# Performance work log

Measured on AMD Instinct MI355X. Metric: run time of the kernel, lower is better.

The kernel has to match this reference:

```python
import jax, jax.numpy as jnp
import numpy as np

# Module hyper-parameters (eval mode: remove_rand_on_eval=True => no random additional points)
B, H, C, E = 2, 8, 2048, 1024
D = 64          # head_size
KP = 8          # k (points per query per head)
P = 2 * KP      # num_points = k * 2**rank, rank = 1


def setup_inputs() -> dict:
    key = jax.random.key(0)
    ks = jax.random.split(key, 10)
    x = jax.random.normal(ks[0], (B, C, E), jnp.float32)
    attention_mask = jnp.ones((B, C), jnp.int32)  # accepted but unused, as in the torch forward
    # hyper() outputs (abstract in the class): continuous means in [0, C-1), positive sigmas, values
    means = jax.random.uniform(ks[1], (B, H, C, KP, 1), jnp.float32) * (C - 1)
    sigmas = jax.random.uniform(ks[2], (B, H, C, KP), jnp.float32) * 2.0 + 0.5
    values = jax.random.normal(ks[3], (B, H, C, KP), jnp.float32)
    s_in = 1.0 / np.sqrt(E).astype(np.float32)
    s_u = 1.0 / np.sqrt(H * D).astype(np.float32)
    Wk = jax.random.normal(ks[4], (E, H * D), jnp.float32) * s_in
    Wq = jax.random.normal(ks[5], (E, H * D), jnp.float32) * s_in
    Wv = jax.random.normal(ks[6], (E, H * D), jnp.float32) * s_in
    Wu = jax.random.normal(ks[7], (H * D, E), jnp.float32) * s_u
    bu = jnp.zeros((E,), jnp.float32)
    return dict(x=x, attention_mask=attention_mask, means=means, sigmas=sigmas,
                values=values, Wk=Wk, Wq=Wq, Wv=Wv, Wu=Wu, bu=bu)


def reference(x, attention_mask, means, sigmas, values, Wk, Wq, Wv, Wu, bu):
    b, c, e = x.shape
    h, d, kp, p = H, D, KP, P

    # ---- ngenerate (eval: only the 2**rank = 2 integer corners per mean, clamped in-range) ----
    m = means[..., 0]                                  # (b,h,c,k)
    i0 = jnp.clip(jnp.floor(m).astype(jnp.int32), 0, c - 1)
    i1 = jnp.clip(i0 + 1, 0, c - 1)
    idx = jnp.stack([i0, i1], axis=-1).reshape(b, h, c, p)   # (b,h,c,P)
    idx_fl = idx.astype(jnp.float32)

    # ---- densities: unnormalized Gaussian of each integer point under each of the k means ----
    diff = idx_fl[..., :, None] - m[..., None, :]            # (b,h,c,P,k)
    dens = jnp.exp(-0.5 * (diff / sigmas[..., None, :]) ** 2)

    # ---- nduplicates: zero densities of repeated index tuples (keep first occurrence) ----
    eq = idx[..., :, None] == idx[..., None, :]              # (b,h,c,P,P)
    earlier = jnp.tril(jnp.ones((p, p), bool), k=-1)         # q < p
    dup = jnp.any(eq & earlier, axis=-1)                     # (b,h,c,P)
    dens = jnp.where(dup[..., None], 0.0, dens)

    # normalize over dim=2 (context), exactly as the torch code does
    dens = dens / (dens.sum(axis=2, keepdims=True) + 1e-8)

    # density-weighted continuous values -> per-point weights
    weights = (values[..., None, :] * dens).sum(axis=-1)     # (b,h,c,P)

    # ---- projections ----
    inv_sqrt_d = 1.0 / np.sqrt(d).astype(np.float32)
    Kt = (x @ Wk).reshape(b, c, h, d).transpose(0, 2, 1, 3) * inv_sqrt_d  # (b,h,c,d)
    Qt = (x @ Wq).reshape(b, c, h, d).transpose(0, 2, 1, 3) * inv_sqrt_d
    Vt = (x @ Wv).reshape(b, c, h, d).transpose(0, 2, 1, 3)

    # ---- gather K/V at the sparse indices ----
    flat = idx.reshape(b, h, c * p, 1)
    Kg = jnp.take_along_axis(Kt, flat, axis=2).reshape(b, h, c, p, d)
    Vg = jnp.take_along_axis(Vt, flat, axis=2).reshape(b, h, c, p, d)

    dots = jnp.einsum('bhcd,bhcpd->bhcp', Qt, Kg)
    new_weights = jax.nn.softmax(weights * dots, axis=-1)    # (b,h,c,P)

    head_reps = jnp.einsum('bhcpd,bhcp->bhcd', Vg, new_weights)
    united = head_reps.transpose(0, 2, 1, 3).reshape(b, c, h * d)
    new_out = united @ Wu + bu

    # ---- scatter-add sparse weights into dense attention matrix ----
    bi = jnp.arange(b)[:, None, None, None]
    hi = jnp.arange(h)[None, :, None, None]
    ci = jnp.arange(c)[None, None, :, None]
    attentions = jnp.zeros((b, h, c, c), jnp.float32).at[bi, hi, ci, idx].add(new_weights)

    return new_out, attentions
```

## Files before the change

kernel.cpp:

```cpp
#include <hip/hip_runtime.h>
#include <math.h>
#include <stdint.h>

#define B_ 2
#define H_ 8
#define C_ 2048
#define E_ 1024
#define D_ 64
#define KP_ 8
#define P_ 16
#define HD_ 512
#define ROWS_ 32768
#define M_ 4096

typedef __bf16 bf16x8 __attribute__((ext_vector_type(8)));
typedef float f32x4 __attribute__((ext_vector_type(4)));
typedef uint16_t u16x8 __attribute__((ext_vector_type(8)));

__device__ inline uint16_t f2bf(float f) {
    union { float f; uint32_t u; } v; v.f = f;
    uint32_t u = v.u + 0x7FFF + ((v.u >> 16) & 1);
    return (uint16_t)(u >> 16);
}
__device__ inline float bf2f(uint16_t h) {
    union { uint32_t u; float f; } v; v.u = ((uint32_t)h) << 16;
    return v.f;
}

__device__ inline void gload16(const uint16_t* g, uint16_t* l) {
    __builtin_amdgcn_global_load_lds(
        (const __attribute__((address_space(1))) void*)g,
        (__attribute__((address_space(3))) void*)l, 16, 0, 0);
}

__global__ __launch_bounds__(256) void convert_x_kernel(
    const float* __restrict__ in, uint16_t* __restrict__ out)
{
    const int i = (blockIdx.x * 256 + threadIdx.x) * 8;
    const float4 a = *(const float4*)(in + i);
    const float4 b = *(const float4*)(in + i + 4);
    u16x8 o;
    o[0] = f2bf(a.x); o[1] = f2bf(a.y); o[2] = f2bf(a.z); o[3] = f2bf(a.w);
    o[4] = f2bf(b.x); o[5] = f2bf(b.y); o[6] = f2bf(b.z); o[7] = f2bf(b.w);
    *(u16x8*)(out + i) = o;
}

__global__ __launch_bounds__(256) void convert_wt_kernel(
    const float* __restrict__ Wq, const float* __restrict__ Wk,
    const float* __restrict__ Wv, const float* __restrict__ Wu,
    uint16_t* __restrict__ Wqt, uint16_t* __restrict__ Wkt,
    uint16_t* __restrict__ Wvt, uint16_t* __restrict__ Wut)
{
    const int z = blockIdx.z;
    const float* in; uint16_t* out; int R, Cc;
    if (z == 0)      { in = Wq; out = Wqt; R = E_;  Cc = HD_; }
    else if (z == 1) { in = Wk; out = Wkt; R = E_;  Cc = HD_; }
    else if (z == 2) { in = Wv; out = Wvt; R = E_;  Cc = HD_; }
    else             { in = Wu; out = Wut; R = HD_; Cc = E_; }
    const int tiles_x = Cc >> 5;
    const int tx = blockIdx.x % tiles_x;
    const int ty = blockIdx.x / tiles_x;
    const int r0 = ty * 32, c0 = tx * 32;
    __shared__ float t[32][33];
    const int lx = threadIdx.x & 31, ly = threadIdx.x >> 5;
#pragma unroll
    for (int i = 0; i < 4; ++i)
        t[ly * 4 + i][lx] = in[(size_t)(r0 + ly * 4 + i) * Cc + c0 + lx];
    __syncthreads();
#pragma unroll
    for (int i = 0; i < 4; ++i)
        out[(size_t)(c0 + ly * 4 + i) * R + r0 + lx] = f2bf(t[lx][ly * 4 + i]);
}

__global__ __launch_bounds__(256) void gemm_qkv_kernel(
    const uint16_t* __restrict__ xb,
    const uint16_t* __restrict__ Wqt, const uint16_t* __restrict__ Wkt,
    const uint16_t* __restrict__ Wvt,
    uint16_t* __restrict__ Qt, uint16_t* __restrict__ Kt,
    uint16_t* __restrict__ Vt)
{
    const int z = blockIdx.z;
    const uint16_t* __restrict__ Wt = (z == 0) ? Wqt : (z == 1) ? Wkt : Wvt;
    uint16_t* __restrict__ Out = (z == 0) ? Qt : (z == 1) ? Kt : Vt;
    const float scale = (z == 2) ? 1.0f : 0.125f;
    const int K = E_;
    const int m0 = blockIdx.y * 128;
    const int n0 = blockIdx.x * 128;

    __shared__ __align__(16) uint16_t As[128 * 32];
    __shared__ __align__(16) uint16_t Bs[128 * 32];

    const int tid = threadIdx.x;
    const int w = tid >> 6, lane = tid & 63;
    const int wm = w & 1, wn = w >> 1;

    f32x4 acc[4][4] = {};

    const int r0s = (w * 2 + 0) * 16 + (lane >> 2);
    const int r1s = (w * 2 + 1) * 16 + (lane >> 2);
    const int ko  = (lane & 3) * 8;
    const uint16_t* gA0 = xb + (size_t)(m0 + r0s) * K + ko;
    const uint16_t* gA1 = xb + (size_t)(m0 + r1s) * K + ko;
    const uint16_t* gB0 = Wt + (size_t)(n0 + r0s) * K + ko;
    const uint16_t* gB1 = Wt + (size_t)(n0 + r1s) * K + ko;
    uint16_t* lA0 = &As[(w * 2 + 0) * 512];
    uint16_t* lA1 = &As[(w * 2 + 1) * 512];
    uint16_t* lB0 = &Bs[(w * 2 + 0) * 512];
    uint16_t* lB1 = &Bs[(w * 2 + 1) * 512];

    const int fr = lane & 15;
    const int fk = (lane >> 4) * 8;

    for (int k0 = 0; k0 < K; k0 += 32) {
        __syncthreads();
        gload16(gA0 + k0, lA0);
        gload16(gA1 + k0, lA1);
        gload16(gB0 + k0, lB0);
        gload16(gB1 + k0, lB1);
        __syncthreads();
        bf16x8 af[4], bf[4];
#pragma unroll
        for (int t = 0; t < 4; ++t) {
            af[t] = *(const bf16x8*)&As[(wm * 64 + t * 16 + fr) * 32 + fk];
            bf[t] = *(const bf16x8*)&Bs[(wn * 64 + t * 16 + fr) * 32 + fk];
        }
#pragma unroll
        for (int mt = 0; mt < 4; ++mt)
#pragma unroll
            for (int nt = 0; nt < 4; ++nt)
                acc[mt][nt] = __builtin_amdgcn_mfma_f32_16x16x32_bf16(
                    af[mt], bf[nt], acc[mt][nt], 0, 0, 0);
    }

#pragma unroll
    for (int mt = 0; mt < 4; ++mt) {
#pragma unroll
        for (int nt = 0; nt < 4; ++nt) {
            const int n = n0 + wn * 64 + nt * 16 + fr;
            const int h = n >> 6, d = n & 63;
#pragma unroll
            for (int r = 0; r < 4; ++r) {
                const int m = m0 + wm * 64 + mt * 16 + (lane >> 4) * 4 + r;
                const int b = m >> 11, c = m & (C_ - 1);
                Out[(((size_t)(b * H_ + h) * C_ + c) << 6) + d] =
                    f2bf(acc[mt][nt][r] * scale);
            }
        }
    }
}

__global__ __launch_bounds__(256) void gemm_out_kernel(
    const uint16_t* __restrict__ U, const uint16_t* __restrict__ Wut,
    const float* __restrict__ bu, float* __restrict__ out)
{
    const int K = HD_;
    const int m0 = blockIdx.y * 128;
    const int n0 = blockIdx.x * 128;

    __shared__ __align__(16) uint16_t As[128 * 32];
    __shared__ __align__(16) uint16_t Bs[128 * 32];

    const int tid = threadIdx.x;
    const int w = tid >> 6, lane = tid & 63;
    const int wm = w & 1, wn = w >> 1;

    f32x4 acc[4][4] = {};

    const int r0s = (w * 2 + 0) * 16 + (lane >> 2);
    const int r1s = (w * 2 + 1) * 16 + (lane >> 2);
    const int ko  = (lane & 3) * 8;
    const uint16_t* gA0 = U + (size_t)(m0 + r0s) * K + ko;
    const uint16_t* gA1 = U + (size_t)(m0 + r1s) * K + ko;
    const uint16_t* gB0 = Wut + (size_t)(n0 + r0s) * K + ko;
    const uint16_t* gB1 = Wut + (size_t)(n0 + r1s) * K + ko;
    uint16_t* lA0 = &As[(w * 2 + 0) * 512];
    uint16_t* lA1 = &As[(w * 2 + 1) * 512];
    uint16_t* lB0 = &Bs[(w * 2 + 0) * 512];
    uint16_t* lB1 = &Bs[(w * 2 + 1) * 512];

    const int fr = lane & 15;
    const int fk = (lane >> 4) * 8;

    for (int k0 = 0; k0 < K; k0 += 32) {
        __syncthreads();
        gload16(gA0 + k0, lA0);
        gload16(gA1 + k0, lA1);
        gload16(gB0 + k0, lB0);
        gload16(gB1 + k0, lB1);
        __syncthreads();
        bf16x8 af[4], bf[4];
#pragma unroll
        for (int t = 0; t < 4; ++t) {
            af[t] = *(const bf16x8*)&As[(wm * 64 + t * 16 + fr) * 32 + fk];
            bf[t] = *(const bf16x8*)&Bs[(wn * 64 + t * 16 + fr) * 32 + fk];
        }
#pragma unroll
        for (int mt = 0; mt < 4; ++mt)
#pragma unroll
            for (int nt = 0; nt < 4; ++nt)
                acc[mt][nt] = __builtin_amdgcn_mfma_f32_16x16x32_bf16(
                    af[mt], bf[nt], acc[mt][nt], 0, 0, 0);
    }

#pragma unroll
    for (int mt = 0; mt < 4; ++mt) {
#pragma unroll
        for (int nt = 0; nt < 4; ++nt) {
            const int n = n0 + wn * 64 + nt * 16 + fr;
            const float bias = bu[n];
#pragma unroll
            for (int r = 0; r < 4; ++r) {
                const int m = m0 + wm * 64 + mt * 16 + (lane >> 4) * 4 + r;
                out[(size_t)m * E_ + n] = acc[mt][nt][r] + bias;
            }
        }
    }
}

__global__ __launch_bounds__(256) void dens_sum_kernel(
    const float* __restrict__ means, const float* __restrict__ sigmas,
    float* __restrict__ S)
{
    const int row = blockIdx.x * 256 + threadIdx.x;
    const int lane = threadIdx.x & 63;
    const int bh = row >> 11;

    const float* mrow = means + (size_t)row * 8;
    const float* srow = sigmas + (size_t)row * 8;
    const float4 ma = *(const float4*)(mrow);
    const float4 mb = *(const float4*)(mrow + 4);
    const float4 sa = *(const float4*)(srow);
    const float4 sb = *(const float4*)(srow + 4);
    const float mm[8] = {ma.x, ma.y, ma.z, ma.w, mb.x, mb.y, mb.z, mb.w};
    const float sg[8] = {sa.x, sa.y, sa.z, sa.w, sb.x, sb.y, sb.z, sb.w};

    int idx[16];
#pragma unroll
    for (int j = 0; j < 8; ++j) {
        int i0 = (int)floorf(mm[j]);
        i0 = min(max(i0, 0), C_ - 1);
        idx[2 * j] = i0;
        idx[2 * j + 1] = min(i0 + 1, C_ - 1);
    }
    unsigned dupm = 0;
#pragma unroll
    for (int p = 1; p < 16; ++p) {
        bool d = false;
#pragma unroll
        for (int q = 0; q < 15; ++q)
            if (q < p) d = d || (idx[q] == idx[p]);
        if (d) dupm |= (1u << p);
    }

#pragma unroll
    for (int p = 0; p < 16; ++p) {
        const float fi = (float)idx[p];
        const bool dup = (dupm >> p) & 1u;
#pragma unroll
        for (int kk = 0; kk < 8; ++kk) {
            const float t = (fi - mm[kk]) / sg[kk];
            float val = dup ? 0.0f : expf(-0.5f * t * t);
#pragma unroll
            for (int off = 1; off < 64; off <<= 1)
                val += __shfl_xor(val, off);
            if (lane == 0)
                atomicAdd(&S[bh * 128 + p * 8 + kk], val);
        }
    }
}

__global__ __launch_bounds__(256) void attn_kernel(
    const float* __restrict__ means, const float* __restrict__ sigmas,
    const float* __restrict__ values, const float* __restrict__ S,
    const uint16_t* __restrict__ Qt, const uint16_t* __restrict__ Kt,
    const uint16_t* __restrict__ Vt, uint16_t* __restrict__ united,
    float* __restrict__ attn)
{
    __shared__ float rowbuf[4][2048];
    const int w = threadIdx.x >> 6;
    const int lane = threadIdx.x & 63;
    const int row = blockIdx.x * 4 + w;
    const int bh = row >> 11;
    const int c = row & (C_ - 1);
    const int b = bh >> 3;
    const int h = bh & 7;

    const float* mrow = means + (size_t)row * 8;
    const float4 ma = *(const float4*)(mrow);
    const float4 mb = *(const float4*)(mrow + 4);
    const float mm[8] = {ma.x, ma.y, ma.z, ma.w, mb.x, mb.y, mb.z, mb.w};

    int idx[16];
#pragma unroll
    for (int j = 0; j < 8; ++j) {
        int i0 = (int)floorf(mm[j]);
        i0 = min(max(i0, 0), C_ - 1);
        idx[2 * j] = i0;
        idx[2 * j + 1] = min(i0 + 1, C_ - 1);
    }

    const int lp = lane & 15;
    int myidx = 0;
#pragma unroll
    for (int q = 0; q < 16; ++q)
        if (q == lp) myidx = idx[q];
    float wp = 0.0f;
    if (lane < 16) {
        bool dup = false;
#pragma unroll
        for (int q = 0; q < 15; ++q)
            dup = dup || ((q < lane) && (idx[q] == myidx));
        if (!dup) {
            const float* srow = sigmas + (size_t)row * 8;
            const float* vrow = values + (size_t)row * 8;
            const float4 sa = *(const float4*)(srow);
            const float4 sb = *(const float4*)(srow + 4);
            const float4 va = *(const float4*)(vrow);
            const float4 vb = *(const float4*)(vrow + 4);
            const float sg[8] = {sa.x, sa.y, sa.z, sa.w, sb.x, sb.y, sb.z, sb.w};
            const float vl[8] = {va.x, va.y, va.z, va.w, vb.x, vb.y, vb.z, vb.w};
            const float* Sp = S + bh * 128 + lane * 8;
            const float4 Sa = *(const float4*)(Sp);
            const float4 Sb = *(const float4*)(Sp + 4);
            const float Sv[8] = {Sa.x, Sa.y, Sa.z, Sa.w, Sb.x, Sb.y, Sb.z, Sb.w};
            const float fi = (float)myidx;
#pragma unroll
            for (int kk = 0; kk < 8; ++kk) {
                const float t = (fi - mm[kk]) / sg[kk];
                const float e = expf(-0.5f * t * t);
                wp = fmaf(vl[kk], e / (Sv[kk] + 1e-8f), wp);
            }
        }
    }

    const int p = lane >> 2, g = lane & 3;
    int kidx = 0;
#pragma unroll
    for (int q = 0; q < 16; ++q)
        if (q == p) kidx = idx[q];

    const uint16_t* Qrow = Qt + ((size_t)row << 6);
    const uint16_t* Krow = Kt + ((((size_t)bh << 11) + kidx) << 6);
    const u16x8 qa = *(const u16x8*)(Qrow + g * 16);
    const u16x8 qb = *(const u16x8*)(Qrow + g * 16 + 8);
    const u16x8 ka = *(const u16x8*)(Krow + g * 16);
    const u16x8 kb = *(const u16x8*)(Krow + g * 16 + 8);
    float dot = 0.0f;
#pragma unroll
    for (int j = 0; j < 8; ++j) {
        dot = fmaf(bf2f(qa[j]), bf2f(ka[j]), dot);
        dot = fmaf(bf2f(qb[j]), bf2f(kb[j]), dot);
    }
    dot += __shfl_xor(dot, 1);
    dot += __shfl_xor(dot, 2);

    const float wvp = __shfl(wp, p);
    const float logit = wvp * dot;

    float mx = logit;
#pragma unroll
    for (int off = 4; off < 64; off <<= 1)
        mx = fmaxf(mx, __shfl_xor(mx, off));
    const float e = expf(logit - mx);
    float se = e;
#pragma unroll
    for (int off = 4; off < 64; off <<= 1)
        se += __shfl_xor(se, off);
    const float sm = e / se;

    float smv[16];
#pragma unroll
    for (int q = 0; q < 16; ++q)
        smv[q] = __shfl(sm, q * 4);

    const uint16_t* Vbh = Vt + ((size_t)bh << 17);
    float acc = 0.0f;
#pragma unroll
    for (int q = 0; q < 16; ++q)
        acc = fmaf(bf2f(Vbh[((size_t)idx[q] << 6) + lane]), smv[q], acc);
    united[((size_t)(b * C_ + c)) * HD_ + h * 64 + lane] = f2bf(acc);

    const float4 z4 = make_float4(0.f, 0.f, 0.f, 0.f);
#pragma unroll
    for (int j = 0; j < 8; ++j)
        *(float4*)&rowbuf[w][(j * 64 + lane) * 4] = z4;
    __syncthreads();
    if (lane < 16) atomicAdd(&rowbuf[w][myidx], smv[lane]);
    __syncthreads();
    float* arow = attn + ((size_t)row << 11);
#pragma unroll
    for (int j = 0; j < 8; ++j) {
        const int o = (j * 64 + lane) * 4;
        *(float4*)&arow[o] = *(const float4*)&rowbuf[w][o];
    }
}

extern "C" void kernel_launch(void* const* d_in, const int* in_sizes, int n_in,
                              void* d_out, int out_size, void* d_ws,
                              size_t ws_size, hipStream_t stream) {
    const float* x      = (const float*)d_in[0];
    const float* means  = (const float*)d_in[2];
    const float* sigmas = (const float*)d_in[3];
    const float* values = (const float*)d_in[4];
    const float* Wk     = (const float*)d_in[5];
    const float* Wq     = (const float*)d_in[6];
    const float* Wv     = (const float*)d_in[7];
    const float* Wu     = (const float*)d_in[8];
    const float* bu     = (const float*)d_in[9];

    float* out  = (float*)d_out;
    float* attn = out + (size_t)M_ * E_;

    uint16_t* wsp = (uint16_t*)d_ws;
    uint16_t* xb     = wsp;
    uint16_t* Wqt    = xb + 4194304;
    uint16_t* Wkt    = Wqt + 524288;
    uint16_t* Wvt    = Wkt + 524288;
    uint16_t* Wut    = Wvt + 524288;
    uint16_t* Qt     = Wut + 524288;
    uint16_t* Kt     = Qt + 2097152;
    uint16_t* Vt     = Kt + 2097152;
    uint16_t* united = Vt + 2097152;
    float*    S      = (float*)(united + 2097152);

    hipMemsetAsync(S, 0, 2048 * sizeof(float), stream);

    convert_x_kernel<<<2048, 256, 0, stream>>>(x, xb);
    convert_wt_kernel<<<dim3(512, 1, 4), 256, 0, stream>>>(
        Wq, Wk, Wv, Wu, Wqt, Wkt, Wvt, Wut);
    dens_sum_kernel<<<128, 256, 0, stream>>>(means, sigmas, S);
    gemm_qkv_kernel<<<dim3(4, 32, 3), 256, 0, stream>>>(
        xb, Wqt, Wkt, Wvt, Qt, Kt, Vt);
    attn_kernel<<<ROWS_ / 4, 256, 0, stream>>>(
        means, sigmas, values, S, Qt, Kt, Vt, united, attn);
    gemm_out_kernel<<<dim3(8, 32), 256, 0, stream>>>(united, Wut, bu, out);
}
```

Before: 423.9 us.

## Fuse QKV weights into one matrix, fold scale, write attention rows directly

The Q/K/V weight transposes are packed into one contiguous matrix, and the 1/sqrt(d) scale is folded into the weight conversion. The QKV GEMM becomes a single 12x32 grid that picks its output buffer from the column tile. The attention kernel drops its 32KB shared-memory row buffer and the two block barriers. It now zeroes each attention row with nontemporal global stores, issues a threadfence, then atomically adds the 16 softmax weights into global memory. This should raise occupancy and remove the LDS staging, but it depends on the zero stores being ordered before the global atomics, and it adds global atomic traffic.

```diff
diff --git a/kernel.cpp b/kernel.cpp
--- a/kernel.cpp
+++ b/kernel.cpp
@@ -48,15 +48,14 @@
 __global__ __launch_bounds__(256) void convert_wt_kernel(
     const float* __restrict__ Wq, const float* __restrict__ Wk,
     const float* __restrict__ Wv, const float* __restrict__ Wu,
-    uint16_t* __restrict__ Wqt, uint16_t* __restrict__ Wkt,
-    uint16_t* __restrict__ Wvt, uint16_t* __restrict__ Wut)
+    uint16_t* __restrict__ Wall, uint16_t* __restrict__ Wut)
 {
     const int z = blockIdx.z;
-    const float* in; uint16_t* out; int R, Cc;
-    if (z == 0)      { in = Wq; out = Wqt; R = E_;  Cc = HD_; }
-    else if (z == 1) { in = Wk; out = Wkt; R = E_;  Cc = HD_; }
-    else if (z == 2) { in = Wv; out = Wvt; R = E_;  Cc = HD_; }
-    else             { in = Wu; out = Wut; R = HD_; Cc = E_; }
+    const float* in; uint16_t* out; int R, Cc; float scale;
+    if (z == 0)      { in = Wq; out = Wall;                 R = E_;  Cc = HD_; scale = 0.125f; }
+    else if (z == 1) { in = Wk; out = Wall + 512 * 1024;    R = E_;  Cc = HD_; scale = 0.125f; }
+    else if (z == 2) { in = Wv; out = Wall + 1024 * 1024;   R = E_;  Cc = HD_; scale = 1.0f; }
+    else             { in = Wu; out = Wut;                  R = HD_; Cc = E_;  scale = 1.0f; }
     const int tiles_x = Cc >> 5;
     const int tx = blockIdx.x % tiles_x;
     const int ty = blockIdx.x / tiles_x;
@@ -69,23 +68,19 @@
     __syncthreads();
 #pragma unroll
     for (int i = 0; i < 4; ++i)
-        out[(size_t)(c0 + ly * 4 + i) * R + r0 + lx] = f2bf(t[lx][ly * 4 + i]);
+        out[(size_t)(c0 + ly * 4 + i) * R + r0 + lx] = f2bf(t[lx][ly * 4 + i] * scale);
 }
 
 __global__ __launch_bounds__(256) void gemm_qkv_kernel(
-    const uint16_t* __restrict__ xb,
-    const uint16_t* __restrict__ Wqt, const uint16_t* __restrict__ Wkt,
-    const uint16_t* __restrict__ Wvt,
+    const uint16_t* __restrict__ xb, const uint16_t* __restrict__ Wall,
     uint16_t* __restrict__ Qt, uint16_t* __restrict__ Kt,
     uint16_t* __restrict__ Vt)
 {
-    const int z = blockIdx.z;
-    const uint16_t* __restrict__ Wt = (z == 0) ? Wqt : (z == 1) ? Wkt : Wvt;
-    uint16_t* __restrict__ Out = (z == 0) ? Qt : (z == 1) ? Kt : Vt;
-    const float scale = (z == 2) ? 1.0f : 0.125f;
     const int K = E_;
     const int m0 = blockIdx.y * 128;
     const int n0 = blockIdx.x * 128;
+    const int z = n0 >> 9;
+    uint16_t* __restrict__ Out = (z == 0) ? Qt : (z == 1) ? Kt : Vt;
 
     __shared__ __align__(16) uint16_t As[128 * 32];
     __shared__ __align__(16) uint16_t Bs[128 * 32];
@@ -101,8 +96,8 @@
     const int ko  = (lane & 3) * 8;
     const uint16_t* gA0 = xb + (size_t)(m0 + r0s) * K + ko;
     const uint16_t* gA1 = xb + (size_t)(m0 + r1s) * K + ko;
-    const uint16_t* gB0 = Wt + (size_t)(n0 + r0s) * K + ko;
-    const uint16_t* gB1 = Wt + (size_t)(n0 + r1s) * K + ko;
+    const uint16_t* gB0 = Wall + (size_t)(n0 + r0s) * K + ko;
+    const uint16_t* gB1 = Wall + (size_t)(n0 + r1s) * K + ko;
     uint16_t* lA0 = &As[(w * 2 + 0) * 512];
     uint16_t* lA1 = &As[(w * 2 + 1) * 512];
     uint16_t* lB0 = &Bs[(w * 2 + 0) * 512];
@@ -136,14 +131,14 @@
     for (int mt = 0; mt < 4; ++mt) {
 #pragma unroll
         for (int nt = 0; nt < 4; ++nt) {
-            const int n = n0 + wn * 64 + nt * 16 + fr;
-            const int h = n >> 6, d = n & 63;
+            const int nl = (n0 & 511) + wn * 64 + nt * 16 + fr;
+            const int h = nl >> 6, d = nl & 63;
 #pragma unroll
             for (int r = 0; r < 4; ++r) {
                 const int m = m0 + wm * 64 + mt * 16 + (lane >> 4) * 4 + r;
                 const int b = m >> 11, c = m & (C_ - 1);
                 Out[(((size_t)(b * H_ + h) * C_ + c) << 6) + d] =
-                    f2bf(acc[mt][nt][r] * scale);
+                    f2bf(acc[mt][nt][r]);
             }
         }
     }
@@ -276,7 +271,6 @@
     const uint16_t* __restrict__ Vt, uint16_t* __restrict__ united,
     float* __restrict__ attn)
 {
-    __shared__ float rowbuf[4][2048];
     const int w = threadIdx.x >> 6;
     const int lane = threadIdx.x & 63;
     const int row = blockIdx.x * 4 + w;
@@ -372,6 +366,7 @@
 #pragma unroll
     for (int q = 0; q < 16; ++q)
         smv[q] = __shfl(sm, q * 4);
+    const float myw = __shfl(sm, lp * 4);
 
     const uint16_t* Vbh = Vt + ((size_t)bh << 17);
     float acc = 0.0f;
@@ -380,19 +375,13 @@
         acc = fmaf(bf2f(Vbh[((size_t)idx[q] << 6) + lane]), smv[q], acc);
     united[((size_t)(b * C_ + c)) * HD_ + h * 64 + lane] = f2bf(acc);
 
-    const float4 z4 = make_float4(0.f, 0.f, 0.f, 0.f);
+    float* arow = attn + ((size_t)row << 11);
+    const f32x4 z4 = {0.f, 0.f, 0.f, 0.f};
 #pragma unroll
     for (int j = 0; j < 8; ++j)
-        *(float4*)&rowbuf[w][(j * 64 + lane) * 4] = z4;
-    __syncthreads();
-    if (lane < 16) atomicAdd(&rowbuf[w][myidx], smv[lane]);
-    __syncthreads();
-    float* arow = attn + ((size_t)row << 11);
-#pragma unroll
-    for (int j = 0; j < 8; ++j) {
-        const int o = (j * 64 + lane) * 4;
-        *(float4*)&arow[o] = *(const float4*)&rowbuf[w][o];
-    }
+        __builtin_nontemporal_store(z4, (f32x4*)&arow[(j * 64 + lane) * 4]);
+    __threadfence();
+    if (lane < 16) atomicAdd(&arow[myidx], myw);
 }
 
 extern "C" void kernel_launch(void* const* d_in, const int* in_sizes, int n_in,
@@ -413,24 +402,21 @@
 
     uint16_t* wsp = (uint16_t*)d_ws;
     uint16_t* xb     = wsp;
-    uint16_t* Wqt    = xb + 4194304;
-    uint16_t* Wkt    = Wqt + 524288;
-    uint16_t* Wvt    = Wkt + 524288;
-    uint16_t* Wut    = Wvt + 524288;
+    uint16_t* Wall   = xb + 4194304;
+    uint16_t* Wut    = Wall + 1572864;
     uint16_t* Qt     = Wut + 524288;
     uint16_t* Kt     = Qt + 2097152;
     uint16_t* Vt     = Kt + 2097152;
     uint16_t* united = Vt + 2097152;
     float*    S      = (float*)(united + 2097152);
 
-    hipMemsetAsync(S, 0, 2048 * sizeof(float), stream);
+    (void)hipMemsetAsync(S, 0, 2048 * sizeof(float), stream);
 
     convert_x_kernel<<<2048, 256, 0, stream>>>(x, xb);
     convert_wt_kernel<<<dim3(512, 1, 4), 256, 0, stream>>>(
-        Wq, Wk, Wv, Wu, Wqt, Wkt, Wvt, Wut);
+        Wq, Wk, Wv, Wu, Wall, Wut);
     dens_sum_kernel<<<128, 256, 0, stream>>>(means, sigmas, S);
-    gemm_qkv_kernel<<<dim3(4, 32, 3), 256, 0, stream>>>(
-        xb, Wqt, Wkt, Wvt, Qt, Kt, Vt);
+    gemm_qkv_kernel<<<dim3(12, 32), 256, 0, stream>>>(xb, Wall, Qt, Kt, Vt);
     attn_kernel<<<ROWS_ / 4, 256, 0, stream>>>(
         means, sigmas, values, S, Qt, Kt, Vt, united, attn);
     gemm_out_kernel<<<dim3(8, 32), 256, 0, stream>>>(united, Wut, bu, out);
```

Result: slower. 1.448 ms (+241.4%).
